# Kernel optimization log

Hardware: AMD Instinct MI355X
Metric: run time of the kernel (lower is better)

The kernel has to match this reference:

```python
import jax, jax.numpy as jnp
import numpy as np

B = 8192
N = 722          # number of independent tiny MLPs
CAM = 10         # CAMERA_VECTOR_DIM
IN = CAM + 1     # per-MLP input dim
H = 10           # hidden dim
LOD = 6          # NUM_LOD_LEVELS


def setup_inputs() -> dict:
    key = jax.random.key(0)
    ks = jax.random.split(key, 8)
    return {
        "prior_lod": jax.random.uniform(ks[0], (B, N), dtype=jnp.float32),
        "camera": jax.random.normal(ks[1], (B, CAM), dtype=jnp.float32),
        "W1": jax.random.normal(ks[2], (N, IN, H), dtype=jnp.float32) * 0.3,
        "b1": jax.random.normal(ks[3], (N, H), dtype=jnp.float32) * 0.1,
        "W2": jax.random.normal(ks[4], (N, H, H), dtype=jnp.float32) * 0.3,
        "b2": jax.random.normal(ks[5], (N, H), dtype=jnp.float32) * 0.1,
        "W3": jax.random.normal(ks[6], (N, H, LOD), dtype=jnp.float32) * 0.3,
        "b3": jax.random.normal(ks[7], (N, LOD), dtype=jnp.float32) * 0.1,
    }


def reference(prior_lod, camera, W1, b1, W2, b2, W3, b3):
    # Per-network input: cat(prior_lod[:, i:i+1], camera) -> [B, N, IN]
    cam = jnp.broadcast_to(camera[:, None, :], (prior_lod.shape[0], W1.shape[0], camera.shape[1]))
    x = jnp.concatenate([prior_lod[:, :, None], cam], axis=-1)  # [B, N, IN]
    # Batched 3-layer MLP over the N axis (grouped GEMM equivalent of the 722-loop)
    h = jax.nn.relu(jnp.einsum('bni,nih->bnh', x, W1) + b1[None])   # [B, N, H]
    h = jax.nn.relu(jnp.einsum('bnh,nhk->bnk', h, W2) + b2[None])   # [B, N, H]
    out = jnp.einsum('bnh,nho->bno', h, W3) + b3[None]              # [B, N, LOD]
    return out  # stacked version of the original list of 722 [B, LOD] outputs
```

## Files before the change

kernel.cpp:

```cpp
#include <hip/hip_runtime.h>


#define NN 722
#define CAMD 10
#define HD 10
#define LODD 6
#define ROWF (NN * LODD)
#define SUB 4
#define BT 256
#define NETS_PER_CHUNK 4
#define NCHUNKS 181
#define CPG 2
#define NGROUPS 91
#define LSTRIDE 25
#define HROWS 128

__global__ __launch_bounds__(256) void Net_18966575579675_kernel(
    const float* __restrict__ prior, const float* __restrict__ camera,
    const float* __restrict__ W1, const float* __restrict__ b1,
    const float* __restrict__ W2, const float* __restrict__ b2,
    const float* __restrict__ W3, const float* __restrict__ b3,
    float* __restrict__ out)
{
    const int tid  = threadIdx.x;
    const int lane = tid & 63;
    const int wave = __builtin_amdgcn_readfirstlane(tid >> 6);
    const int b0   = blockIdx.x * BT;

    const int c_begin = blockIdx.y * CPG;
    const int c_end   = (c_begin + CPG < NCHUNKS) ? (c_begin + CPG) : NCHUNKS;

    __shared__ float lds[HROWS * LSTRIDE];

    float cam[SUB][CAMD];
#pragma unroll
    for (int s = 0; s < SUB; ++s) {
        const float2* cam2 = (const float2*)(camera + (size_t)(b0 + s * 64 + lane) * CAMD);
#pragma unroll
        for (int i = 0; i < CAMD / 2; ++i) {
            float2 v = cam2[i];
            cam[s][2 * i]     = v.x;
            cam[s][2 * i + 1] = v.y;
        }
    }

    for (int c = c_begin; c < c_end; ++c) {
        const int n = c * NETS_PER_CHUNK + wave;

        float o[SUB][LODD];
        if (n < NN) {
            const float* __restrict__ w1 = W1 + (size_t)n * (CAMD + 1) * HD;
            const float* __restrict__ p1 = b1 + (size_t)n * HD;
            const float* __restrict__ w2 = W2 + (size_t)n * HD * HD;
            const float* __restrict__ p2 = b2 + (size_t)n * HD;
            const float* __restrict__ w3 = W3 + (size_t)n * HD * LODD;
            const float* __restrict__ p3 = b3 + (size_t)n * LODD;

            float pr[SUB];
#pragma unroll
            for (int s = 0; s < SUB; ++s)
                pr[s] = prior[(size_t)(b0 + s * 64 + lane) * NN + n];

            float h1[SUB][HD];
#pragma unroll
            for (int j = 0; j < HD; ++j) {
                const float bj = p1[j];
                const float w  = w1[j];
#pragma unroll
                for (int s = 0; s < SUB; ++s)
                    h1[s][j] = fmaf(pr[s], w, bj);
            }
#pragma unroll
            for (int i = 0; i < CAMD; ++i) {
#pragma unroll
                for (int j = 0; j < HD; ++j) {
                    const float w = w1[(i + 1) * HD + j];
#pragma unroll
                    for (int s = 0; s < SUB; ++s)
                        h1[s][j] = fmaf(cam[s][i], w, h1[s][j]);
                }
            }
#pragma unroll
            for (int s = 0; s < SUB; ++s)
#pragma unroll
                for (int j = 0; j < HD; ++j)
                    h1[s][j] = fmaxf(h1[s][j], 0.0f);

            float h2[SUB][HD];
#pragma unroll
            for (int k = 0; k < HD; ++k) {
                const float bk = p2[k];
#pragma unroll
                for (int s = 0; s < SUB; ++s)
                    h2[s][k] = bk;
            }
#pragma unroll
            for (int j = 0; j < HD; ++j) {
#pragma unroll
                for (int k = 0; k < HD; ++k) {
                    const float w = w2[j * HD + k];
#pragma unroll
                    for (int s = 0; s < SUB; ++s)
                        h2[s][k] = fmaf(h1[s][j], w, h2[s][k]);
                }
            }
#pragma unroll
            for (int s = 0; s < SUB; ++s)
#pragma unroll
                for (int k = 0; k < HD; ++k)
                    h2[s][k] = fmaxf(h2[s][k], 0.0f);

#pragma unroll
            for (int m = 0; m < LODD; ++m) {
                const float bm = p3[m];
#pragma unroll
                for (int s = 0; s < SUB; ++s)
                    o[s][m] = bm;
            }
#pragma unroll
            for (int j = 0; j < HD; ++j) {
#pragma unroll
                for (int m = 0; m < LODD; ++m) {
                    const float w = w3[j * LODD + m];
#pragma unroll
                    for (int s = 0; s < SUB; ++s)
                        o[s][m] = fmaf(h2[s][j], w, o[s][m]);
                }
            }
        }

        const int rem = NN - c * NETS_PER_CHUNK;
        const int nv  = rem < NETS_PER_CHUNK ? rem : NETS_PER_CHUNK;

#pragma unroll
        for (int p = 0; p < 2; ++p) {
            if (n < NN) {
#pragma unroll
                for (int ss = 0; ss < 2; ++ss)
#pragma unroll
                    for (int m = 0; m < LODD; ++m)
                        lds[(ss * 64 + lane) * LSTRIDE + wave * LODD + m] = o[2 * p + ss][m];
            }
            __syncthreads();

            if (nv == NETS_PER_CHUNK) {
                for (int f = tid; f < HROWS * 6; f += 256) {
                    const int row  = f / 6;
                    const int colq = f - row * 6;
                    const float* s = lds + row * LSTRIDE + colq * 4;
                    float4 v = make_float4(s[0], s[1], s[2], s[3]);
                    *(float4*)(out + (size_t)(b0 + p * HROWS + row) * ROWF
                               + c * (NETS_PER_CHUNK * LODD) + colq * 4) = v;
                }
            } else {
                for (int f = tid; f < HROWS * 3; f += 256) {
                    const int row  = f / 3;
                    const int colq = f - row * 3;
                    const float* s = lds + row * LSTRIDE + colq * 4;
                    float4 v = make_float4(s[0], s[1], s[2], s[3]);
                    *(float4*)(out + (size_t)(b0 + p * HROWS + row) * ROWF
                               + c * (NETS_PER_CHUNK * LODD) + colq * 4) = v;
                }
            }
            __syncthreads();
        }
    }
}

extern "C" void kernel_launch(void* const* d_in, const int* in_sizes, int n_in,
                              void* d_out, int out_size, void* d_ws, size_t ws_size,
                              hipStream_t stream) {
    const float* prior  = (const float*)d_in[0];
    const float* camera = (const float*)d_in[1];
    const float* W1     = (const float*)d_in[2];
    const float* b1     = (const float*)d_in[3];
    const float* W2     = (const float*)d_in[4];
    const float* b2     = (const float*)d_in[5];
    const float* W3     = (const float*)d_in[6];
    const float* b3     = (const float*)d_in[7];
    float* out = (float*)d_out;

    dim3 grid(8192 / BT, NGROUPS);
    dim3 block(256);
    Net_18966575579675_kernel<<<grid, block, 0, stream>>>(
        prior, camera, W1, b1, W2, b2, W3, b3, out);
}
```

Before: 260.4 us.

## Double-buffer LDS staging, prefetch next chunk's prior, use lighter barriers

The LDS staging buffer becomes double-buffered, so the trailing barrier after each output write phase is removed and the next phase writes into the other buffer. The prior values for the next chunk are loaded while the current chunk computes, hiding global load latency. __syncthreads is replaced by an explicit lgkmcnt wait plus s_barrier, so outstanding global stores are not waited on at each barrier. This costs twice the LDS and a few more registers, and it relies on the alternating buffers being enough to avoid read/write races across phases.

```diff
diff --git a/kernel.cpp b/kernel.cpp
--- a/kernel.cpp
+++ b/kernel.cpp
@@ -15,6 +15,11 @@
 #define LSTRIDE 25
 #define HROWS 128
 
+__device__ __forceinline__ void lds_barrier() {
+    asm volatile("s_waitcnt lgkmcnt(0)" ::: "memory");
+    __builtin_amdgcn_s_barrier();
+}
+
 __global__ __launch_bounds__(256) void Net_18966575579675_kernel(
     const float* __restrict__ prior, const float* __restrict__ camera,
     const float* __restrict__ W1, const float* __restrict__ b1,
@@ -30,7 +35,7 @@
     const int c_begin = blockIdx.y * CPG;
     const int c_end   = (c_begin + CPG < NCHUNKS) ? (c_begin + CPG) : NCHUNKS;
 
-    __shared__ float lds[HROWS * LSTRIDE];
+    __shared__ float lds[2][HROWS * LSTRIDE];
 
     float cam[SUB][CAMD];
 #pragma unroll
@@ -44,8 +49,28 @@
         }
     }
 
+    float pr[SUB];
+    {
+        const int n0 = c_begin * NETS_PER_CHUNK + wave;
+        const int nc = n0 < NN ? n0 : NN - 1;
+#pragma unroll
+        for (int s = 0; s < SUB; ++s)
+            pr[s] = prior[(size_t)(b0 + s * 64 + lane) * NN + nc];
+    }
+
+    int g = 0;
+
     for (int c = c_begin; c < c_end; ++c) {
         const int n = c * NETS_PER_CHUNK + wave;
+
+        float prn[SUB];
+        if (c + 1 < c_end) {
+            const int n1 = (c + 1) * NETS_PER_CHUNK + wave;
+            const int nc = n1 < NN ? n1 : NN - 1;
+#pragma unroll
+            for (int s = 0; s < SUB; ++s)
+                prn[s] = prior[(size_t)(b0 + s * 64 + lane) * NN + nc];
+        }
 
         float o[SUB][LODD];
         if (n < NN) {
@@ -56,11 +81,6 @@
             const float* __restrict__ w3 = W3 + (size_t)n * HD * LODD;
             const float* __restrict__ p3 = b3 + (size_t)n * LODD;
 
-            float pr[SUB];
-#pragma unroll
-            for (int s = 0; s < SUB; ++s)
-                pr[s] = prior[(size_t)(b0 + s * 64 + lane) * NN + n];
-
             float h1[SUB][HD];
 #pragma unroll
             for (int j = 0; j < HD; ++j) {
@@ -134,20 +154,21 @@
 
 #pragma unroll
         for (int p = 0; p < 2; ++p) {
+            float* lbuf = lds[g];
             if (n < NN) {
 #pragma unroll
                 for (int ss = 0; ss < 2; ++ss)
 #pragma unroll
                     for (int m = 0; m < LODD; ++m)
-                        lds[(ss * 64 + lane) * LSTRIDE + wave * LODD + m] = o[2 * p + ss][m];
-            }
-            __syncthreads();
+                        lbuf[(ss * 64 + lane) * LSTRIDE + wave * LODD + m] = o[2 * p + ss][m];
+            }
+            lds_barrier();
 
             if (nv == NETS_PER_CHUNK) {
                 for (int f = tid; f < HROWS * 6; f += 256) {
                     const int row  = f / 6;
                     const int colq = f - row * 6;
-                    const float* s = lds + row * LSTRIDE + colq * 4;
+                    const float* s = lbuf + row * LSTRIDE + colq * 4;
                     float4 v = make_float4(s[0], s[1], s[2], s[3]);
                     *(float4*)(out + (size_t)(b0 + p * HROWS + row) * ROWF
                                + c * (NETS_PER_CHUNK * LODD) + colq * 4) = v;
@@ -156,14 +177,18 @@
                 for (int f = tid; f < HROWS * 3; f += 256) {
                     const int row  = f / 3;
                     const int colq = f - row * 3;
-                    const float* s = lds + row * LSTRIDE + colq * 4;
+                    const float* s = lbuf + row * LSTRIDE + colq * 4;
                     float4 v = make_float4(s[0], s[1], s[2], s[3]);
                     *(float4*)(out + (size_t)(b0 + p * HROWS + row) * ROWF
                                + c * (NETS_PER_CHUNK * LODD) + colq * 4) = v;
                 }
             }
-            __syncthreads();
-        }
+            g ^= 1;
+        }
+
+#pragma unroll
+        for (int s = 0; s < SUB; ++s)
+            pr[s] = prn[s];
     }
 }
 
```

Result: faster. 250.0 us (-4.0%).

## Stage camera in LDS, process sub-rows sequentially, prefetch prior values

Applied to the files above, without the earlier changes.

Camera vectors now sit in shared memory instead of 40 registers per thread. The MLP is evaluated one sub-row at a time in a non-unrolled loop rather than four at once, which cuts register pressure so more waves can be resident. The next chunk's prior values are prefetched during the current chunk, and __syncthreads is replaced with an explicit lgkmcnt wait plus s_barrier. In exchange, weights are reloaded per sub-row (scalar loads), the four-way register reuse of each weight is lost, and there are extra LDS reads of the camera.

```diff
diff --git a/kernel.cpp b/kernel.cpp
--- a/kernel.cpp
+++ b/kernel.cpp
@@ -15,6 +15,11 @@
 #define LSTRIDE 25
 #define HROWS 128
 
+__device__ __forceinline__ void lds_barrier() {
+    asm volatile("s_waitcnt lgkmcnt(0)" ::: "memory");
+    __builtin_amdgcn_s_barrier();
+}
+
 __global__ __launch_bounds__(256) void Net_18966575579675_kernel(
     const float* __restrict__ prior, const float* __restrict__ camera,
     const float* __restrict__ W1, const float* __restrict__ b1,
@@ -30,140 +35,137 @@
     const int c_begin = blockIdx.y * CPG;
     const int c_end   = (c_begin + CPG < NCHUNKS) ? (c_begin + CPG) : NCHUNKS;
 
-    __shared__ float lds[HROWS * LSTRIDE];
+    __shared__ float cam_lds[CAMD][BT];
+    __shared__ float obuf[HROWS * LSTRIDE];
 
-    float cam[SUB][CAMD];
-#pragma unroll
-    for (int s = 0; s < SUB; ++s) {
-        const float2* cam2 = (const float2*)(camera + (size_t)(b0 + s * 64 + lane) * CAMD);
+    {
+        const float2* c2 = (const float2*)(camera + (size_t)(b0 + tid) * CAMD);
 #pragma unroll
         for (int i = 0; i < CAMD / 2; ++i) {
-            float2 v = cam2[i];
-            cam[s][2 * i]     = v.x;
-            cam[s][2 * i + 1] = v.y;
+            float2 v = c2[i];
+            cam_lds[2 * i][tid]     = v.x;
+            cam_lds[2 * i + 1][tid] = v.y;
         }
     }
 
+    float pr0, pr1, pr2, pr3;
+    {
+        const int n0 = c_begin * NETS_PER_CHUNK + wave;
+        const int nc = n0 < NN ? n0 : NN - 1;
+        pr0 = prior[(size_t)(b0 + 0 * 64 + lane) * NN + nc];
+        pr1 = prior[(size_t)(b0 + 1 * 64 + lane) * NN + nc];
+        pr2 = prior[(size_t)(b0 + 2 * 64 + lane) * NN + nc];
+        pr3 = prior[(size_t)(b0 + 3 * 64 + lane) * NN + nc];
+    }
+
+    lds_barrier();
+
     for (int c = c_begin; c < c_end; ++c) {
-        const int n = c * NETS_PER_CHUNK + wave;
+        const int n   = c * NETS_PER_CHUNK + wave;
+        const bool act = (n < NN);
+        const int nc  = act ? n : NN - 1;
 
-        float o[SUB][LODD];
-        if (n < NN) {
-            const float* __restrict__ w1 = W1 + (size_t)n * (CAMD + 1) * HD;
-            const float* __restrict__ p1 = b1 + (size_t)n * HD;
-            const float* __restrict__ w2 = W2 + (size_t)n * HD * HD;
-            const float* __restrict__ p2 = b2 + (size_t)n * HD;
-            const float* __restrict__ w3 = W3 + (size_t)n * HD * LODD;
-            const float* __restrict__ p3 = b3 + (size_t)n * LODD;
+        const float* __restrict__ w1 = W1 + (size_t)nc * (CAMD + 1) * HD;
+        const float* __restrict__ p1 = b1 + (size_t)nc * HD;
+        const float* __restrict__ w2 = W2 + (size_t)nc * HD * HD;
+        const float* __restrict__ p2 = b2 + (size_t)nc * HD;
+        const float* __restrict__ w3 = W3 + (size_t)nc * HD * LODD;
+        const float* __restrict__ p3 = b3 + (size_t)nc * LODD;
 
-            float pr[SUB];
-#pragma unroll
-            for (int s = 0; s < SUB; ++s)
-                pr[s] = prior[(size_t)(b0 + s * 64 + lane) * NN + n];
-
-            float h1[SUB][HD];
-#pragma unroll
-            for (int j = 0; j < HD; ++j) {
-                const float bj = p1[j];
-                const float w  = w1[j];
-#pragma unroll
-                for (int s = 0; s < SUB; ++s)
-                    h1[s][j] = fmaf(pr[s], w, bj);
-            }
-#pragma unroll
-            for (int i = 0; i < CAMD; ++i) {
-#pragma unroll
-                for (int j = 0; j < HD; ++j) {
-                    const float w = w1[(i + 1) * HD + j];
-#pragma unroll
-                    for (int s = 0; s < SUB; ++s)
-                        h1[s][j] = fmaf(cam[s][i], w, h1[s][j]);
-                }
-            }
-#pragma unroll
-            for (int s = 0; s < SUB; ++s)
-#pragma unroll
-                for (int j = 0; j < HD; ++j)
-                    h1[s][j] = fmaxf(h1[s][j], 0.0f);
-
-            float h2[SUB][HD];
-#pragma unroll
-            for (int k = 0; k < HD; ++k) {
-                const float bk = p2[k];
-#pragma unroll
-                for (int s = 0; s < SUB; ++s)
-                    h2[s][k] = bk;
-            }
-#pragma unroll
-            for (int j = 0; j < HD; ++j) {
-#pragma unroll
-                for (int k = 0; k < HD; ++k) {
-                    const float w = w2[j * HD + k];
-#pragma unroll
-                    for (int s = 0; s < SUB; ++s)
-                        h2[s][k] = fmaf(h1[s][j], w, h2[s][k]);
-                }
-            }
-#pragma unroll
-            for (int s = 0; s < SUB; ++s)
-#pragma unroll
-                for (int k = 0; k < HD; ++k)
-                    h2[s][k] = fmaxf(h2[s][k], 0.0f);
-
-#pragma unroll
-            for (int m = 0; m < LODD; ++m) {
-                const float bm = p3[m];
-#pragma unroll
-                for (int s = 0; s < SUB; ++s)
-                    o[s][m] = bm;
-            }
-#pragma unroll
-            for (int j = 0; j < HD; ++j) {
-#pragma unroll
-                for (int m = 0; m < LODD; ++m) {
-                    const float w = w3[j * LODD + m];
-#pragma unroll
-                    for (int s = 0; s < SUB; ++s)
-                        o[s][m] = fmaf(h2[s][j], w, o[s][m]);
-                }
-            }
+        float prn0 = pr0, prn1 = pr1, prn2 = pr2, prn3 = pr3;
+        if (c + 1 < c_end) {
+            const int n1 = (c + 1) * NETS_PER_CHUNK + wave;
+            const int nx = n1 < NN ? n1 : NN - 1;
+            prn0 = prior[(size_t)(b0 + 0 * 64 + lane) * NN + nx];
+            prn1 = prior[(size_t)(b0 + 1 * 64 + lane) * NN + nx];
+            prn2 = prior[(size_t)(b0 + 2 * 64 + lane) * NN + nx];
+            prn3 = prior[(size_t)(b0 + 3 * 64 + lane) * NN + nx];
         }
 
         const int rem = NN - c * NETS_PER_CHUNK;
         const int nv  = rem < NETS_PER_CHUNK ? rem : NETS_PER_CHUNK;
 
+#pragma unroll 1
+        for (int s = 0; s < SUB; ++s) {
+            if (act) {
+                const int row = s * 64 + lane;
+                const float prs = (s == 0) ? pr0 : (s == 1) ? pr1
+                                  : (s == 2) ? pr2 : pr3;
+
+                float cv[CAMD];
 #pragma unroll
-        for (int p = 0; p < 2; ++p) {
-            if (n < NN) {
+                for (int i = 0; i < CAMD; ++i)
+                    cv[i] = cam_lds[i][row];
+
+                float h1[HD];
 #pragma unroll
-                for (int ss = 0; ss < 2; ++ss)
+                for (int j = 0; j < HD; ++j)
+                    h1[j] = fmaf(prs, w1[j], p1[j]);
+#pragma unroll
+                for (int i = 0; i < CAMD; ++i)
+#pragma unroll
+                    for (int j = 0; j < HD; ++j)
+                        h1[j] = fmaf(cv[i], w1[(i + 1) * HD + j], h1[j]);
+#pragma unroll
+                for (int j = 0; j < HD; ++j)
+                    h1[j] = fmaxf(h1[j], 0.0f);
+
+                float h2[HD];
+#pragma unroll
+                for (int k = 0; k < HD; ++k)
+                    h2[k] = p2[k];
+#pragma unroll
+                for (int j = 0; j < HD; ++j)
+#pragma unroll
+                    for (int k = 0; k < HD; ++k)
+                        h2[k] = fmaf(h1[j], w2[j * HD + k], h2[k]);
+#pragma unroll
+                for (int k = 0; k < HD; ++k)
+                    h2[k] = fmaxf(h2[k], 0.0f);
+
+                float o[LODD];
+#pragma unroll
+                for (int m = 0; m < LODD; ++m)
+                    o[m] = p3[m];
+#pragma unroll
+                for (int j = 0; j < HD; ++j)
 #pragma unroll
                     for (int m = 0; m < LODD; ++m)
-                        lds[(ss * 64 + lane) * LSTRIDE + wave * LODD + m] = o[2 * p + ss][m];
+                        o[m] = fmaf(h2[j], w3[j * LODD + m], o[m]);
+
+                const int lrow = (s & 1) * 64 + lane;
+#pragma unroll
+                for (int m = 0; m < LODD; ++m)
+                    obuf[lrow * LSTRIDE + wave * LODD + m] = o[m];
             }
-            __syncthreads();
 
-            if (nv == NETS_PER_CHUNK) {
-                for (int f = tid; f < HROWS * 6; f += 256) {
-                    const int row  = f / 6;
-                    const int colq = f - row * 6;
-                    const float* s = lds + row * LSTRIDE + colq * 4;
-                    float4 v = make_float4(s[0], s[1], s[2], s[3]);
-                    *(float4*)(out + (size_t)(b0 + p * HROWS + row) * ROWF
-                               + c * (NETS_PER_CHUNK * LODD) + colq * 4) = v;
+            if (s & 1) {
+                lds_barrier();
+                const int h = s >> 1;
+                if (nv == NETS_PER_CHUNK) {
+                    for (int f = tid; f < HROWS * 6; f += 256) {
+                        const int row  = f / 6;
+                        const int colq = f - row * 6;
+                        const float* sp = obuf + row * LSTRIDE + colq * 4;
+                        float4 v = make_float4(sp[0], sp[1], sp[2], sp[3]);
+                        *(float4*)(out + (size_t)(b0 + h * HROWS + row) * ROWF
+                                   + c * (NETS_PER_CHUNK * LODD) + colq * 4) = v;
+                    }
+                } else {
+                    for (int f = tid; f < HROWS * 3; f += 256) {
+                        const int row  = f / 3;
+                        const int colq = f - row * 3;
+                        const float* sp = obuf + row * LSTRIDE + colq * 4;
+                        float4 v = make_float4(sp[0], sp[1], sp[2], sp[3]);
+                        *(float4*)(out + (size_t)(b0 + h * HROWS + row) * ROWF
+                                   + c * (NETS_PER_CHUNK * LODD) + colq * 4) = v;
+                    }
                 }
-            } else {
-                for (int f = tid; f < HROWS * 3; f += 256) {
-                    const int row  = f / 3;
-                    const int colq = f - row * 3;
-                    const float* s = lds + row * LSTRIDE + colq * 4;
-                    float4 v = make_float4(s[0], s[1], s[2], s[3]);
-                    *(float4*)(out + (size_t)(b0 + p * HROWS + row) * ROWF
-                               + c * (NETS_PER_CHUNK * LODD) + colq * 4) = v;
-                }
+                lds_barrier();
             }
-            __syncthreads();
         }
+
+        pr0 = prn0; pr1 = prn1; pr2 = prn2; pr3 = prn3;
     }
 }
 
```

Result: faster. 250.4 us (-3.8%).
